# Optimization experiments

Measured on AMD Instinct MI355X. Metric: run time of the kernel, lower is better.

## Reference

```python
import jax, jax.numpy as jnp
import numpy as np

ENC_H = 128
DEC_H = 256
DEC_STEPS = 10


def _gru_cell(x, h, Wih, Whh, bih, bhh):
    # PyTorch GRU cell, gate order (r, z, n)
    gi = x @ Wih.T + bih          # (B, 3H)
    gh = h @ Whh.T + bhh          # (B, 3H)
    H = h.shape[-1]
    ir, iz, inn = gi[:, :H], gi[:, H:2 * H], gi[:, 2 * H:]
    hr, hz, hn = gh[:, :H], gh[:, H:2 * H], gh[:, 2 * H:]
    r = jax.nn.sigmoid(ir + hr)
    z = jax.nn.sigmoid(iz + hz)
    n = jnp.tanh(inn + r * hn)
    return (1.0 - z) * n + z * h


def setup_inputs() -> dict:
    key = jax.random.key(0)
    ks = jax.random.split(key, 12)
    B, S = 4096, 128
    s = 0.1
    return {
        "x": jax.random.normal(ks[0], (B, S, 5), jnp.float32),
        "y": jax.random.normal(ks[1], (B, S, 1), jnp.float32),
        "enc_Wih": jax.random.normal(ks[2], (3 * ENC_H, 5), jnp.float32) * s,
        "enc_Whh": jax.random.normal(ks[3], (3 * ENC_H, ENC_H), jnp.float32) * s,
        "enc_bih": jax.random.normal(ks[4], (3 * ENC_H,), jnp.float32) * s,
        "enc_bhh": jax.random.normal(ks[5], (3 * ENC_H,), jnp.float32) * s,
        "dec_Wih": jax.random.normal(ks[6], (3 * DEC_H, ENC_H + 1), jnp.float32) * s,
        "dec_Whh": jax.random.normal(ks[7], (3 * DEC_H, DEC_H), jnp.float32) * s,
        "dec_bih": jax.random.normal(ks[8], (3 * DEC_H,), jnp.float32) * s,
        "dec_bhh": jax.random.normal(ks[9], (3 * DEC_H,), jnp.float32) * s,
        "lin_W": jax.random.normal(ks[10], (4, DEC_H), jnp.float32) * s,
        "lin_b": jax.random.normal(ks[11], (4,), jnp.float32) * s,
    }


def reference(x, y, enc_Wih, enc_Whh, enc_bih, enc_bhh,
              dec_Wih, dec_Whh, dec_bih, dec_bhh, lin_W, lin_b):
    B, S, _ = x.shape
    xs = jnp.transpose(x, (1, 0, 2))   # (S, B, 5)
    ys = jnp.transpose(y, (1, 0, 2))   # (S, B, 1)

    # Encoder: only the final hidden state (contex) is consumed downstream.
    h0 = jnp.zeros((B, ENC_H), x.dtype)

    def enc_step(h, xt):
        return _gru_cell(xt, h, enc_Wih, enc_Whh, enc_bih, enc_bhh), None

    contex, _ = jax.lax.scan(enc_step, h0, xs)   # (B, 128)

    # Decoder: initial hidden is ones (torch.ones_like(shape)), 10 steps.
    hdec0 = jnp.ones((B, DEC_H), x.dtype)

    def dec_step(h, yt):
        xt = jnp.concatenate([contex, yt], axis=-1)   # (B, 129)
        h2 = _gru_cell(xt, h, dec_Wih, dec_Whh, dec_bih, dec_bhh)
        out = h2 @ lin_W.T + lin_b                    # (B, 4)
        return h2, out

    _, outs = jax.lax.scan(dec_step, hdec0, ys[:DEC_STEPS])  # (10, B, 4)

    # res starts as ones; only first 10 rows written.
    res = jnp.ones((S, B, 4), x.dtype).at[:DEC_STEPS].set(outs)
    return jnp.transpose(res, (1, 0, 2))   # (B, S, 4)
```

## Files before the change

### kernel.cpp

```cpp
#include <hip/hip_runtime.h>

#define B_SZ 4096
#define S_SZ 128
#define XD 5
#define EH 128
#define DH 256
#define DSTEPS 10

typedef short v8s __attribute__((ext_vector_type(8)));
typedef float v4f __attribute__((ext_vector_type(4)));

__device__ __forceinline__ float bf2f(unsigned short u) {
    union { unsigned int i; float f; } v; v.i = ((unsigned int)u) << 16; return v.f;
}
__device__ __forceinline__ unsigned short f2bf(float f) {
    union { float f; unsigned int i; } v; v.f = f;
    unsigned int x = v.i;
    return (unsigned short)((x + 0x7FFFu + ((x >> 16) & 1u)) >> 16);
}
__device__ __forceinline__ float fexp2(float x) { return __builtin_amdgcn_exp2f(x); }
__device__ __forceinline__ float frcp(float x) { return __builtin_amdgcn_rcpf(x); }
__device__ __forceinline__ float sigmoidf_(float x) {
    return frcp(1.f + fexp2(-1.44269504088896f * x));
}
__device__ __forceinline__ float tanhf_(float x) {
    float e = fexp2(2.88539008177793f * x);
    return 1.f - 2.f * frcp(e + 1.f);
}

__global__ __launch_bounds__(512) void enc_kernel(
    const float* __restrict__ x,
    const float* __restrict__ Wih32,
    const float* __restrict__ Whh32,
    const float* __restrict__ bih,
    const float* __restrict__ bhh,
    const float* __restrict__ dWih,
    const float* __restrict__ dWhh,
    unsigned short* __restrict__ wihp,
    unsigned short* __restrict__ dWhh_bf,
    unsigned short* __restrict__ ctex)
{
    __shared__ unsigned short xs[S_SZ][16][8];
    __shared__ unsigned short hb[2][16][136];
    __shared__ unsigned short zpad[8];

    const int tid = threadIdx.x;
    const int bid = blockIdx.x;
    const int wv = tid >> 6;
    const int lane = tid & 63;
    const int n = lane & 15;
    const int kg = lane >> 4;
    const int r0 = bid * 16;

    for (int i = bid * 512 + tid; i < 768 * 256; i += 131072)
        dWhh_bf[i] = f2bf(dWhh[i]);
    for (int i = bid * 512 + tid; i < 768 * 136; i += 131072) {
        int col = i / 136, k = i - col * 136;
        wihp[i] = (k < 129) ? f2bf(dWih[col * 129 + k]) : (unsigned short)0;
    }

    for (int i = tid; i < 2 * 16 * 136; i += 512) ((unsigned short*)hb)[i] = 0;
    if (tid < 8) zpad[tid] = 0;
    for (int i = tid; i < 16 * S_SZ * 8; i += 512) {
        int m = i >> 10;
        int rem = i & 1023;
        int t = rem >> 3;
        int j = rem & 7;
        unsigned short v = 0;
        if (j < XD) v = f2bf(x[(size_t)(r0 + m) * (S_SZ * XD) + t * XD + j]);
        xs[t][m][j] = v;
    }

    const int colw = wv * 16 + n;
    v8s fw[3][4];
    v8s fx[3];
    #pragma unroll
    for (int g = 0; g < 3; ++g) {
        int gcol = g * EH + colw;
        #pragma unroll
        for (int kt = 0; kt < 4; ++kt) {
            const float* p = &Whh32[(size_t)gcol * EH + kt * 32 + kg * 8];
            float4 lo = *(const float4*)p;
            float4 hi = *(const float4*)(p + 4);
            v8s f;
            f[0] = (short)f2bf(lo.x); f[1] = (short)f2bf(lo.y);
            f[2] = (short)f2bf(lo.z); f[3] = (short)f2bf(lo.w);
            f[4] = (short)f2bf(hi.x); f[5] = (short)f2bf(hi.y);
            f[6] = (short)f2bf(hi.z); f[7] = (short)f2bf(hi.w);
            fw[g][kt] = f;
        }
        v8s t = {0, 0, 0, 0, 0, 0, 0, 0};
        if (kg == 0) {
            const float* p = &Wih32[gcol * XD];
            #pragma unroll
            for (int j = 0; j < XD; ++j) t[j] = (short)f2bf(p[j]);
        }
        fx[g] = t;
    }
    const float b_r  = bih[colw]          + bhh[colw];
    const float b_z  = bih[EH + colw]     + bhh[EH + colw];
    const float bi_n = bih[2 * EH + colw];
    const float bh_n = bhh[2 * EH + colw];

    float hst[4] = {0.f, 0.f, 0.f, 0.f};
    __syncthreads();

    #pragma unroll 2
    for (int t = 0; t < S_SZ; ++t) {
        const int p = t & 1;
        v8s a[4];
        #pragma unroll
        for (int kt = 0; kt < 4; ++kt)
            a[kt] = *(const v8s*)&hb[p][n][kt * 32 + kg * 8];
        const unsigned short* xsrc = (kg == 0) ? &xs[t][n][0] : &zpad[0];
        v8s ax = *(const v8s*)xsrc;

        v4f accr  = {b_r, b_r, b_r, b_r};
        v4f accz  = {b_z, b_z, b_z, b_z};
        v4f acchn = {bh_n, bh_n, bh_n, bh_n};
        v4f accin = {bi_n, bi_n, bi_n, bi_n};
        #pragma unroll
        for (int kt = 0; kt < 4; ++kt) {
            accr  = __builtin_amdgcn_mfma_f32_16x16x32_bf16(a[kt], fw[0][kt], accr, 0, 0, 0);
            accz  = __builtin_amdgcn_mfma_f32_16x16x32_bf16(a[kt], fw[1][kt], accz, 0, 0, 0);
            acchn = __builtin_amdgcn_mfma_f32_16x16x32_bf16(a[kt], fw[2][kt], acchn, 0, 0, 0);
        }
        accr  = __builtin_amdgcn_mfma_f32_16x16x32_bf16(ax, fx[0], accr, 0, 0, 0);
        accz  = __builtin_amdgcn_mfma_f32_16x16x32_bf16(ax, fx[1], accz, 0, 0, 0);
        accin = __builtin_amdgcn_mfma_f32_16x16x32_bf16(ax, fx[2], accin, 0, 0, 0);

        #pragma unroll
        for (int e = 0; e < 4; ++e) {
            float r = sigmoidf_(accr[e]);
            float z = sigmoidf_(accz[e]);
            float nn = tanhf_(accin[e] + r * acchn[e]);
            float h = (1.f - z) * nn + z * hst[e];
            hst[e] = h;
            hb[1 - p][kg * 4 + e][colw] = f2bf(h);
        }
        __syncthreads();
    }
    #pragma unroll
    for (int e = 0; e < 4; ++e)
        ctex[(size_t)(r0 + kg * 4 + e) * EH + colw] = f2bf(hst[e]);
}

__global__ __launch_bounds__(512)
__attribute__((amdgpu_waves_per_eu(2, 2)))
void dec_all_kernel(
    const unsigned short* __restrict__ dWhh_bf,
    const unsigned short* __restrict__ wihp,
    const float* __restrict__ dbih,
    const float* __restrict__ dbhh,
    const float* __restrict__ y,
    const unsigned short* __restrict__ ctex,
    const float* __restrict__ linW,
    const float* __restrict__ linb,
    float* __restrict__ out)
{
    __shared__ unsigned short wshn[32 * 264 * 8];
    __shared__ unsigned short hshf[32 * 16 * 8];
    __shared__ unsigned short lwf[32 * 16 * 8];

    const int tid  = threadIdx.x;
    const int w    = tid >> 6;
    const int lane = tid & 63;
    const int n    = lane & 15;
    const int kg   = lane >> 4;
    const int rb   = blockIdx.x * 16;
    const int cbase = w * 32;

    for (int i = tid; i < 256 * 32; i += 512) {
        int col = i >> 5, kgrp = i & 31;
        uint4 v = *(const uint4*)&dWhh_bf[(size_t)(512 + col) * 256 + kgrp * 8];
        *(uint4*)&wshn[(kgrp * 264 + col) * 8] = v;
    }
    {
        int col = tid >> 5, kgrp = tid & 31;
        unsigned short v8[8];
        #pragma unroll
        for (int j = 0; j < 8; ++j)
            v8[j] = (col < 4) ? f2bf(linW[col * 256 + kgrp * 8 + j]) : (unsigned short)0;
        *(uint4*)&lwf[(kgrp * 16 + col) * 8] = *(uint4*)v8;
    }
    for (int i = tid; i < 32 * 16 * 8; i += 512) hshf[i] = 0x3F80;

    v8s fB[2][2][8];
    #pragma unroll
    for (int g = 0; g < 2; ++g)
        #pragma unroll
        for (int cg = 0; cg < 2; ++cg)
            #pragma unroll
            for (int kt = 0; kt < 8; ++kt)
                fB[g][cg][kt] = *(const v8s*)
                    &dWhh_bf[(size_t)(g * DH + cbase + cg * 16 + n) * DH + kt * 32 + kg * 8];

    v4f gi[3][2];
    float wy[3][2], bNh[2];
    #pragma unroll
    for (int g = 0; g < 3; ++g)
        #pragma unroll
        for (int cg = 0; cg < 2; ++cg) {
            int gcol = g * DH + cbase + cg * 16 + n;
            float bb = dbih[gcol] + ((g < 2) ? dbhh[gcol] : 0.f);
            gi[g][cg] = (v4f){bb, bb, bb, bb};
            wy[g][cg] = bf2f(wihp[(size_t)gcol * 136 + 128]);
        }
    #pragma unroll
    for (int cg = 0; cg < 2; ++cg)
        bNh[cg] = dbhh[2 * DH + cbase + cg * 16 + n];

    #pragma unroll
    for (int kt = 0; kt < 4; ++kt) {
        v8s a = *(const v8s*)&ctex[(size_t)(rb + n) * EH + kt * 32 + kg * 8];
        #pragma unroll
        for (int g = 0; g < 3; ++g)
            #pragma unroll
            for (int cg = 0; cg < 2; ++cg) {
                v8s b = *(const v8s*)
                    &wihp[(size_t)(g * DH + cbase + cg * 16 + n) * 136 + kt * 32 + kg * 8];
                gi[g][cg] = __builtin_amdgcn_mfma_f32_16x16x32_bf16(a, b, gi[g][cg], 0, 0, 0);
            }
    }

    const float lb = (n < 4) ? linb[n] : 0.f;
    float hprev[2][4];
    #pragma unroll
    for (int cg = 0; cg < 2; ++cg)
        #pragma unroll
        for (int e = 0; e < 4; ++e) hprev[cg][e] = 1.0f;

    __syncthreads();

    for (int t = 0; t < DSTEPS; ++t) {
        float yv[4];
        #pragma unroll
        for (int e = 0; e < 4; ++e)
            yv[e] = y[(size_t)(rb + kg * 4 + e) * S_SZ + t];

        v4f ar[2], az[2], an[2];
        #pragma unroll
        for (int cg = 0; cg < 2; ++cg) {
            ar[cg] = (v4f){0.f, 0.f, 0.f, 0.f};
            az[cg] = (v4f){0.f, 0.f, 0.f, 0.f};
            an[cg] = (v4f){bNh[cg], bNh[cg], bNh[cg], bNh[cg]};
        }
        #pragma unroll
        for (int kt = 0; kt < 8; ++kt) {
            v8s a = *(const v8s*)&hshf[((kt * 4 + kg) * 16 + n) * 8];
            #pragma unroll
            for (int cg = 0; cg < 2; ++cg) {
                v8s bn_ = *(const v8s*)&wshn[((kt * 4 + kg) * 264 + cbase + cg * 16 + n) * 8];
                ar[cg] = __builtin_amdgcn_mfma_f32_16x16x32_bf16(a, fB[0][cg][kt], ar[cg], 0, 0, 0);
                az[cg] = __builtin_amdgcn_mfma_f32_16x16x32_bf16(a, fB[1][cg][kt], az[cg], 0, 0, 0);
                an[cg] = __builtin_amdgcn_mfma_f32_16x16x32_bf16(a, bn_,           an[cg], 0, 0, 0);
            }
        }
        __syncthreads();

        #pragma unroll
        for (int cg = 0; cg < 2; ++cg) {
            const int chi = 4 * w + 2 * cg + (n >> 3);
            #pragma unroll
            for (int e = 0; e < 4; ++e) {
                float r  = sigmoidf_(gi[0][cg][e] + yv[e] * wy[0][cg] + ar[cg][e]);
                float z  = sigmoidf_(gi[1][cg][e] + yv[e] * wy[1][cg] + az[cg][e]);
                float nn = tanhf_(gi[2][cg][e] + yv[e] * wy[2][cg] + r * an[cg][e]);
                float h  = nn + z * (hprev[cg][e] - nn);
                hprev[cg][e] = h;
                hshf[(chi * 16 + kg * 4 + e) * 8 + (n & 7)] = f2bf(h);
            }
        }
        __syncthreads();

        if (w == 0) {
            v4f o4 = {0.f, 0.f, 0.f, 0.f};
            #pragma unroll
            for (int kt = 0; kt < 8; ++kt) {
                v8s a = *(const v8s*)&hshf[((kt * 4 + kg) * 16 + n) * 8];
                v8s b = *(const v8s*)&lwf[((kt * 4 + kg) * 16 + n) * 8];
                o4 = __builtin_amdgcn_mfma_f32_16x16x32_bf16(a, b, o4, 0, 0, 0);
            }
            if (n < 4) {
                #pragma unroll
                for (int e = 0; e < 4; ++e)
                    out[(size_t)(rb + kg * 4 + e) * (S_SZ * 4) + t * 4 + n] = o4[e] + lb;
            }
        }
    }

    for (int j = tid; j < 16 * 512; j += 512) {
        int row = j >> 9, c = j & 511;
        if (c >= DSTEPS * 4) out[(size_t)(rb + row) * 512 + c] = 1.0f;
    }
}

extern "C" void kernel_launch(void* const* d_in, const int* in_sizes, int n_in,
                              void* d_out, int out_size, void* d_ws, size_t ws_size,
                              hipStream_t stream)
{
    const float* x    = (const float*)d_in[0];
    const float* y    = (const float*)d_in[1];
    const float* eWih = (const float*)d_in[2];
    const float* eWhh = (const float*)d_in[3];
    const float* ebih = (const float*)d_in[4];
    const float* ebhh = (const float*)d_in[5];
    const float* dWih = (const float*)d_in[6];
    const float* dWhh = (const float*)d_in[7];
    const float* dbih = (const float*)d_in[8];
    const float* dbhh = (const float*)d_in[9];
    const float* linW = (const float*)d_in[10];
    const float* linb = (const float*)d_in[11];
    float* out = (float*)d_out;

    char* ws = (char*)d_ws;
    unsigned short* wihp    = (unsigned short*)(ws);
    unsigned short* dWhh_bf = (unsigned short*)(ws + 208896);
    unsigned short* ctex    = (unsigned short*)(ws + 602112);

    enc_kernel<<<256, 512, 0, stream>>>(x, eWih, eWhh, ebih, ebhh,
                                        dWih, dWhh, wihp, dWhh_bf, ctex);
    dec_all_kernel<<<256, 512, 0, stream>>>(dWhh_bf, wihp, dbih, dbhh, y,
                                            ctex, linW, linb, out);
}
```

Before: 217.4 us.

## Fuse encoder and decoder GRU kernels into a single kernel

Merges the encoder and decoder kernels into one launch. The encoder's final hidden state stays in shared memory and feeds the decoder's input projection directly, so the context no longer makes a round trip through global memory. The shared-memory buffer for the staged x sequence is reused for the decoder's n-gate weights. The separate pass that converted decoder weights to bf16 in a workspace is removed: each block now reads fp32 weights and converts them itself. This saves a launch and a global round trip, but every block repeats the weight conversion and reads fp32 data with an unaligned stride of 129. The fused kernel's register and occupancy limits now also apply to the encoder phase.

```diff
diff --git a/kernel.cpp b/kernel.cpp
--- a/kernel.cpp
+++ b/kernel.cpp
@@ -27,40 +27,60 @@
     float e = fexp2(2.88539008177793f * x);
     return 1.f - 2.f * frcp(e + 1.f);
 }
-
-__global__ __launch_bounds__(512) void enc_kernel(
+__device__ __forceinline__ v8s pack8(const float* p) {
+    v8s f;
+    f[0] = (short)f2bf(p[0]); f[1] = (short)f2bf(p[1]);
+    f[2] = (short)f2bf(p[2]); f[3] = (short)f2bf(p[3]);
+    f[4] = (short)f2bf(p[4]); f[5] = (short)f2bf(p[5]);
+    f[6] = (short)f2bf(p[6]); f[7] = (short)f2bf(p[7]);
+    return f;
+}
+
+__global__ __launch_bounds__(512)
+__attribute__((amdgpu_waves_per_eu(2, 2)))
+void fused_kernel(
     const float* __restrict__ x,
-    const float* __restrict__ Wih32,
-    const float* __restrict__ Whh32,
-    const float* __restrict__ bih,
-    const float* __restrict__ bhh,
+    const float* __restrict__ eWih,
+    const float* __restrict__ eWhh,
+    const float* __restrict__ ebih,
+    const float* __restrict__ ebhh,
     const float* __restrict__ dWih,
     const float* __restrict__ dWhh,
-    unsigned short* __restrict__ wihp,
-    unsigned short* __restrict__ dWhh_bf,
-    unsigned short* __restrict__ ctex)
+    const float* __restrict__ dbih,
+    const float* __restrict__ dbhh,
+    const float* __restrict__ y,
+    const float* __restrict__ linW,
+    const float* __restrict__ linb,
+    float* __restrict__ out)
 {
-    __shared__ unsigned short xs[S_SZ][16][8];
+    __shared__ unsigned short ureg[32 * 264 * 8];
     __shared__ unsigned short hb[2][16][136];
+    __shared__ unsigned short hshf[32 * 16 * 8];
+    __shared__ unsigned short lwf[32 * 16 * 8];
     __shared__ unsigned short zpad[8];
+
+    unsigned short (*xs)[16][8] = (unsigned short (*)[16][8])ureg;
+    unsigned short* wshn = ureg;
 
     const int tid = threadIdx.x;
     const int bid = blockIdx.x;
-    const int wv = tid >> 6;
+    const int w = tid >> 6;
     const int lane = tid & 63;
     const int n = lane & 15;
     const int kg = lane >> 4;
     const int r0 = bid * 16;
 
-    for (int i = bid * 512 + tid; i < 768 * 256; i += 131072)
-        dWhh_bf[i] = f2bf(dWhh[i]);
-    for (int i = bid * 512 + tid; i < 768 * 136; i += 131072) {
-        int col = i / 136, k = i - col * 136;
-        wihp[i] = (k < 129) ? f2bf(dWih[col * 129 + k]) : (unsigned short)0;
-    }
-
     for (int i = tid; i < 2 * 16 * 136; i += 512) ((unsigned short*)hb)[i] = 0;
     if (tid < 8) zpad[tid] = 0;
+    for (int i = tid; i < 32 * 16 * 8; i += 512) hshf[i] = 0x3F80;
+    {
+        int col = tid >> 5, kgrp = tid & 31;
+        unsigned short v8[8];
+        #pragma unroll
+        for (int j = 0; j < 8; ++j)
+            v8[j] = (col < 4) ? f2bf(linW[col * 256 + kgrp * 8 + j]) : (unsigned short)0;
+        *(uint4*)&lwf[(kgrp * 16 + col) * 8] = *(uint4*)v8;
+    }
     for (int i = tid; i < 16 * S_SZ * 8; i += 512) {
         int m = i >> 10;
         int rem = i & 1023;
@@ -71,36 +91,27 @@
         xs[t][m][j] = v;
     }
 
-    const int colw = wv * 16 + n;
+    const int colw = w * 16 + n;
     v8s fw[3][4];
     v8s fx[3];
     #pragma unroll
     for (int g = 0; g < 3; ++g) {
         int gcol = g * EH + colw;
         #pragma unroll
-        for (int kt = 0; kt < 4; ++kt) {
-            const float* p = &Whh32[(size_t)gcol * EH + kt * 32 + kg * 8];
-            float4 lo = *(const float4*)p;
-            float4 hi = *(const float4*)(p + 4);
-            v8s f;
-            f[0] = (short)f2bf(lo.x); f[1] = (short)f2bf(lo.y);
-            f[2] = (short)f2bf(lo.z); f[3] = (short)f2bf(lo.w);
-            f[4] = (short)f2bf(hi.x); f[5] = (short)f2bf(hi.y);
-            f[6] = (short)f2bf(hi.z); f[7] = (short)f2bf(hi.w);
-            fw[g][kt] = f;
-        }
+        for (int kt = 0; kt < 4; ++kt)
+            fw[g][kt] = pack8(&eWhh[(size_t)gcol * EH + kt * 32 + kg * 8]);
         v8s t = {0, 0, 0, 0, 0, 0, 0, 0};
         if (kg == 0) {
-            const float* p = &Wih32[gcol * XD];
+            const float* p = &eWih[gcol * XD];
             #pragma unroll
             for (int j = 0; j < XD; ++j) t[j] = (short)f2bf(p[j]);
         }
         fx[g] = t;
     }
-    const float b_r  = bih[colw]          + bhh[colw];
-    const float b_z  = bih[EH + colw]     + bhh[EH + colw];
-    const float bi_n = bih[2 * EH + colw];
-    const float bh_n = bhh[2 * EH + colw];
+    const float b_r  = ebih[colw]          + ebhh[colw];
+    const float b_z  = ebih[EH + colw]     + ebhh[EH + colw];
+    const float bi_n = ebih[2 * EH + colw];
+    const float bh_n = ebhh[2 * EH + colw];
 
     float hst[4] = {0.f, 0.f, 0.f, 0.f};
     __syncthreads();
@@ -140,50 +151,17 @@
         }
         __syncthreads();
     }
-    #pragma unroll
-    for (int e = 0; e < 4; ++e)
-        ctex[(size_t)(r0 + kg * 4 + e) * EH + colw] = f2bf(hst[e]);
-}
-
-__global__ __launch_bounds__(512)
-__attribute__((amdgpu_waves_per_eu(2, 2)))
-void dec_all_kernel(
-    const unsigned short* __restrict__ dWhh_bf,
-    const unsigned short* __restrict__ wihp,
-    const float* __restrict__ dbih,
-    const float* __restrict__ dbhh,
-    const float* __restrict__ y,
-    const unsigned short* __restrict__ ctex,
-    const float* __restrict__ linW,
-    const float* __restrict__ linb,
-    float* __restrict__ out)
-{
-    __shared__ unsigned short wshn[32 * 264 * 8];
-    __shared__ unsigned short hshf[32 * 16 * 8];
-    __shared__ unsigned short lwf[32 * 16 * 8];
-
-    const int tid  = threadIdx.x;
-    const int w    = tid >> 6;
-    const int lane = tid & 63;
-    const int n    = lane & 15;
-    const int kg   = lane >> 4;
-    const int rb   = blockIdx.x * 16;
+
     const int cbase = w * 32;
 
     for (int i = tid; i < 256 * 32; i += 512) {
         int col = i >> 5, kgrp = i & 31;
-        uint4 v = *(const uint4*)&dWhh_bf[(size_t)(512 + col) * 256 + kgrp * 8];
-        *(uint4*)&wshn[(kgrp * 264 + col) * 8] = v;
-    }
-    {
-        int col = tid >> 5, kgrp = tid & 31;
         unsigned short v8[8];
-        #pragma unroll
-        for (int j = 0; j < 8; ++j)
-            v8[j] = (col < 4) ? f2bf(linW[col * 256 + kgrp * 8 + j]) : (unsigned short)0;
-        *(uint4*)&lwf[(kgrp * 16 + col) * 8] = *(uint4*)v8;
-    }
-    for (int i = tid; i < 32 * 16 * 8; i += 512) hshf[i] = 0x3F80;
+        const float* src = &dWhh[(size_t)(512 + col) * 256 + kgrp * 8];
+        #pragma unroll
+        for (int j = 0; j < 8; ++j) v8[j] = f2bf(src[j]);
+        *(uint4*)&wshn[(kgrp * 264 + col) * 8] = *(uint4*)v8;
+    }
 
     v8s fB[2][2][8];
     #pragma unroll
@@ -192,8 +170,8 @@
         for (int cg = 0; cg < 2; ++cg)
             #pragma unroll
             for (int kt = 0; kt < 8; ++kt)
-                fB[g][cg][kt] = *(const v8s*)
-                    &dWhh_bf[(size_t)(g * DH + cbase + cg * 16 + n) * DH + kt * 32 + kg * 8];
+                fB[g][cg][kt] = pack8(
+                    &dWhh[(size_t)(g * DH + cbase + cg * 16 + n) * DH + kt * 32 + kg * 8]);
 
     v4f gi[3][2];
     float wy[3][2], bNh[2];
@@ -204,7 +182,7 @@
             int gcol = g * DH + cbase + cg * 16 + n;
             float bb = dbih[gcol] + ((g < 2) ? dbhh[gcol] : 0.f);
             gi[g][cg] = (v4f){bb, bb, bb, bb};
-            wy[g][cg] = bf2f(wihp[(size_t)gcol * 136 + 128]);
+            wy[g][cg] = dWih[(size_t)gcol * 129 + 128];
         }
     #pragma unroll
     for (int cg = 0; cg < 2; ++cg)
@@ -212,17 +190,18 @@
 
     #pragma unroll
     for (int kt = 0; kt < 4; ++kt) {
-        v8s a = *(const v8s*)&ctex[(size_t)(rb + n) * EH + kt * 32 + kg * 8];
+        v8s a = *(const v8s*)&hb[0][n][kt * 32 + kg * 8];
         #pragma unroll
         for (int g = 0; g < 3; ++g)
             #pragma unroll
             for (int cg = 0; cg < 2; ++cg) {
-                v8s b = *(const v8s*)
-                    &wihp[(size_t)(g * DH + cbase + cg * 16 + n) * 136 + kt * 32 + kg * 8];
+                v8s b = pack8(
+                    &dWih[(size_t)(g * DH + cbase + cg * 16 + n) * 129 + kt * 32 + kg * 8]);
                 gi[g][cg] = __builtin_amdgcn_mfma_f32_16x16x32_bf16(a, b, gi[g][cg], 0, 0, 0);
             }
     }
 
+    const int rb = r0;
     const float lb = (n < 4) ? linb[n] : 0.f;
     float hprev[2][4];
     #pragma unroll
@@ -232,6 +211,7 @@
 
     __syncthreads();
 
+    #pragma clang loop unroll(disable)
     for (int t = 0; t < DSTEPS; ++t) {
         float yv[4];
         #pragma unroll
@@ -247,14 +227,15 @@
         }
         #pragma unroll
         for (int kt = 0; kt < 8; ++kt) {
-            v8s a = *(const v8s*)&hshf[((kt * 4 + kg) * 16 + n) * 8];
-            #pragma unroll
-            for (int cg = 0; cg < 2; ++cg) {
-                v8s bn_ = *(const v8s*)&wshn[((kt * 4 + kg) * 264 + cbase + cg * 16 + n) * 8];
-                ar[cg] = __builtin_amdgcn_mfma_f32_16x16x32_bf16(a, fB[0][cg][kt], ar[cg], 0, 0, 0);
-                az[cg] = __builtin_amdgcn_mfma_f32_16x16x32_bf16(a, fB[1][cg][kt], az[cg], 0, 0, 0);
-                an[cg] = __builtin_amdgcn_mfma_f32_16x16x32_bf16(a, bn_,           an[cg], 0, 0, 0);
-            }
+            v8s a   = *(const v8s*)&hshf[((kt * 4 + kg) * 16 + n) * 8];
+            v8s bn0 = *(const v8s*)&wshn[((kt * 4 + kg) * 264 + cbase + n) * 8];
+            v8s bn1 = *(const v8s*)&wshn[((kt * 4 + kg) * 264 + cbase + 16 + n) * 8];
+            ar[0] = __builtin_amdgcn_mfma_f32_16x16x32_bf16(a, fB[0][0][kt], ar[0], 0, 0, 0);
+            az[0] = __builtin_amdgcn_mfma_f32_16x16x32_bf16(a, fB[1][0][kt], az[0], 0, 0, 0);
+            an[0] = __builtin_amdgcn_mfma_f32_16x16x32_bf16(a, bn0,         an[0], 0, 0, 0);
+            ar[1] = __builtin_amdgcn_mfma_f32_16x16x32_bf16(a, fB[0][1][kt], ar[1], 0, 0, 0);
+            az[1] = __builtin_amdgcn_mfma_f32_16x16x32_bf16(a, fB[1][1][kt], az[1], 0, 0, 0);
+            an[1] = __builtin_amdgcn_mfma_f32_16x16x32_bf16(a, bn1,         an[1], 0, 0, 0);
         }
         __syncthreads();
 
@@ -313,13 +294,7 @@
     const float* linb = (const float*)d_in[11];
     float* out = (float*)d_out;
 
-    char* ws = (char*)d_ws;
-    unsigned short* wihp    = (unsigned short*)(ws);
-    unsigned short* dWhh_bf = (unsigned short*)(ws + 208896);
-    unsigned short* ctex    = (unsigned short*)(ws + 602112);
-
-    enc_kernel<<<256, 512, 0, stream>>>(x, eWih, eWhh, ebih, ebhh,
-                                        dWih, dWhh, wihp, dWhh_bf, ctex);
-    dec_all_kernel<<<256, 512, 0, stream>>>(dWhh_bf, wihp, dbih, dbhh, y,
-                                            ctex, linW, linb, out);
-}
+    fused_kernel<<<256, 512, 0, stream>>>(x, eWih, eWhh, ebih, ebhh,
+                                          dWih, dWhh, dbih, dbhh, y,
+                                          linW, linb, out);
+}
```

New measurement: 259.8 us. +19.5%, slower.
